# Kernel optimization log

Measured on AMD Instinct MI355X. Metric: run time of the kernel, lower is better.

The kernel has to match this reference:

```python
import jax, jax.numpy as jnp
import numpy as np
import math

B, H, T, N = 2, 4, 2048, 2048
THETA = 2.0 ** 16


def get_freqs(n: int, theta: float) -> jnp.ndarray:
    # quantize arange to multiples of 2, matching torch (t/2).floor()*2
    t = jnp.arange(n, dtype=jnp.float32)
    q = jnp.floor(t / 2.0) * 2.0
    return 1.0 / theta ** (q / n) / (2.0 * math.pi)


def rope(phases: jnp.ndarray, v: jnp.ndarray) -> jnp.ndarray:
    # v: [B,H,T,N]; phases: [T,N] (broadcast). Interleaved pair rotation.
    ph = (phases % 1.0) * (2.0 * math.pi)
    c, s = jnp.cos(ph), jnp.sin(ph)
    v2 = v.reshape(*v.shape[:-1], -1, 2)           # [...,N/2,2]
    v_rot = jnp.stack((-v2[..., 1], v2[..., 0]), axis=-1).reshape(v.shape)
    return (v * c + v_rot * s).astype(v.dtype)


def setup_inputs() -> dict:
    key = jax.random.key(0)
    kq, kv = jax.random.split(key)
    Q = jax.random.normal(kq, (B, H, T, N), dtype=jnp.float32)
    V = jax.random.normal(kv, (B, H, T, N), dtype=jnp.float32)
    return {"Q": Q, "V": V}


def reference(Q, V):
    Tlen = Q.shape[2]
    n = Q.shape[3]
    freqs = get_freqs(n, THETA)                               # [N]
    phases = jnp.arange(Tlen, dtype=jnp.float32)[:, None] * freqs[None, :]  # [T,N]
    QR = rope(phases, Q)                                      # K is Q -> KR = QR
    scores = jnp.einsum('bhtn,bhsn->bhts', QR, QR)            # [B,H,T,T]
    # strictly-causal mask: keep s < t (tril with diagonal=-1)
    mask = jnp.tril(jnp.ones((Tlen, Tlen), dtype=bool), k=-1)
    scores = jnp.where(mask, scores, 0.0)
    out = jnp.einsum('bhts,bhsn->bhtn', scores, V)
    return out
```

## Files before the change

kernel.cpp:

```cpp
#include <hip/hip_runtime.h>
#include <hip/hip_bf16.h>

#define TDIM 2048
#define NDIM 2048
#define BHN  8
#define LD   2048

typedef __attribute__((ext_vector_type(8))) short bf16x8;
typedef __attribute__((ext_vector_type(4))) float f32x4;
typedef unsigned short us;

static __device__ __forceinline__ us f2bf(float x) {
  union { __hip_bfloat16 h; us u; } cv;
  cv.h = __float2bfloat16(x);
  return cv.u;
}

__global__ __launch_bounds__(256) void rope_kernel(const float* __restrict__ Q,
                                                   us* __restrict__ QR,
                                                   int total8) {
  int idx = blockIdx.x * blockDim.x + threadIdx.x;
  if (idx >= total8) return;
  long base = (long)idx * 8;
  int n = (int)(base & (NDIM - 1));
  int t = (int)((base >> 11) & (TDIM - 1));
  const float4* p = reinterpret_cast<const float4*>(Q + base);
  float4 v0 = p[0], v1 = p[1];
  float q[8] = {v0.x, v0.y, v0.z, v0.w, v1.x, v1.y, v1.z, v1.w};
  us r[8];
  float tf = (float)t;
#pragma unroll
  for (int pr = 0; pr < 4; ++pr) {
    int nn = n + pr * 2;
    float freq = __builtin_exp2f((float)nn * (-1.0f / 128.0f)) * 0.15915494309189535f;
    float ph = tf * freq;
    ph = ph - __builtin_floorf(ph);
    float c = __builtin_amdgcn_cosf(ph);
    float s = __builtin_amdgcn_sinf(ph);
    float e = q[2 * pr], o = q[2 * pr + 1];
    r[2 * pr]     = f2bf(e * c - o * s);
    r[2 * pr + 1] = f2bf(o * c + e * s);
  }
  union { us usv[8]; bf16x8 v; } pk;
#pragma unroll
  for (int i = 0; i < 8; ++i) pk.usv[i] = r[i];
  *reinterpret_cast<bf16x8*>(QR + base) = pk.v;
}

__global__ __launch_bounds__(256) void vtrans_kernel(const float* __restrict__ V,
                                                     us* __restrict__ VT,
                                                     us* __restrict__ Sflag) {
  __shared__ float tile[32][33];
  if (Sflag != nullptr && blockIdx.x == 0 && blockIdx.y == 0 && blockIdx.z == 0 &&
      threadIdx.x == 0 && threadIdx.y == 0) {
    for (int h = 0; h < BHN; ++h) {
      unsigned* f = (unsigned*)(Sflag + (long)h * TDIM * LD + 1792);
      for (int i = 0; i < 40; ++i)
        __hip_atomic_store(&f[i], 0u, __ATOMIC_RELAXED, __HIP_MEMORY_SCOPE_AGENT);
    }
  }
  int bh = blockIdx.z;
  int n0 = blockIdx.x * 32, t0 = blockIdx.y * 32;
  const float* Vp = V + (long)bh * TDIM * NDIM;
  us* Tp = VT + (long)bh * TDIM * NDIM;
  int tx = threadIdx.x, ty = threadIdx.y;
#pragma unroll
  for (int i = 0; i < 4; ++i)
    tile[ty + i * 8][tx] = Vp[(long)(t0 + ty + i * 8) * NDIM + n0 + tx];
  __syncthreads();
#pragma unroll
  for (int i = 0; i < 4; ++i)
    Tp[(long)(n0 + ty + i * 8) * TDIM + t0 + tx] = f2bf(tile[tx][ty + i * 8]);
}

template <int PASS>
__device__ __forceinline__ void run_tile(const us* __restrict__ A,
                                         const us* __restrict__ B,
                                         void* __restrict__ Cbase,
                                         us* __restrict__ lds,
                                         int rt, int ct, int tid,
                                         unsigned* __restrict__ fh) {
  const int lane = tid & 63, wid = tid >> 6;
  const int wr = wid >> 2, wc = wid & 3;
  const int l15 = lane & 15, l4 = lane >> 4;
  const int row0 = rt * 256, col0 = ct * 256;
  const int kts = (PASS == 0) ? 32 : (rt + 1) * 4;
  const int fbase = rt * (rt + 1) / 2;

  if constexpr (PASS == 1) {
    if (wid == 0) {
      unsigned need = (1u << (rt + 1)) - 1u;
      for (;;) {
        unsigned ok = 0;
        if (lane <= rt)
          ok = (__hip_atomic_fetch_add(&fh[fbase + lane], 0u, __ATOMIC_RELAXED,
                                       __HIP_MEMORY_SCOPE_AGENT) != 0u);
        unsigned long long m = __ballot(ok);
        if (((unsigned)m & need) == need) break;
        __builtin_amdgcn_s_sleep(8);
      }
    }
    __builtin_amdgcn_s_barrier();
    asm volatile("" ::: "memory");
  }

  f32x4 acc[8][4];
#pragma unroll
  for (int m = 0; m < 8; ++m)
#pragma unroll
    for (int n = 0; n < 4; ++n) acc[m][n] = (f32x4){0.f, 0.f, 0.f, 0.f};

  auto stage = [&](int half , int t) {
    const us* g0 = (half < 2) ? A : B;
    const int tr0 = (half < 2) ? row0 : col0;
    const int h = half & 1;
    us* lb = lds + ((half < 2) ? 0 : 32768) + (t & 1) * 16384;
    const int k0 = t * 64;
#pragma unroll
    for (int r = 0; r < 2; ++r) {
      int off = r * 512 + tid;
      int row = off >> 3;
      int ch = off & 7;
      int chl = ch ^ (row & 7);
      const us* g = g0 + (long)(tr0 + h * 128 + row) * LD + (k0 + chl * 8);
      us* l = lb + h * 8192 + off * 8;
      __builtin_amdgcn_global_load_lds(
          (const __attribute__((address_space(1))) unsigned int*)g,
          (__attribute__((address_space(3))) unsigned int*)l, 16, 0, 0);
    }
  };
  auto ldA = [&](int b, int m, int ks) -> bf16x8 {
    int row = wr * 128 + m * 16 + l15;
    int ch = (ks * 4 + l4) ^ (row & 7);
    return *reinterpret_cast<const bf16x8*>(lds + b * 16384 + row * 64 + ch * 8);
  };
  auto ldB = [&](int b, int n, int ks) -> bf16x8 {
    int row = wc * 64 + n * 16 + l15;
    int ch = (ks * 4 + l4) ^ (row & 7);
    return *reinterpret_cast<const bf16x8*>(lds + 32768 + b * 16384 + row * 64 + ch * 8);
  };

  stage(0, 0); stage(1, 0); stage(2, 0); stage(3, 0);
  if (1 < kts) { stage(2, 1); stage(3, 1); }
  asm volatile("s_waitcnt vmcnt(4)" ::: "memory");
  __builtin_amdgcn_s_barrier();
  __builtin_amdgcn_sched_barrier(0);

  bf16x8 af[4][2], bfr[4][2];
  for (int t = 0; t < kts; ++t) {
    const int b = t & 1;
#pragma unroll
    for (int m = 0; m < 4; ++m) { af[m][0] = ldA(b, m, 0); af[m][1] = ldA(b, m, 1); }
#pragma unroll
    for (int n = 0; n < 2; ++n) { bfr[n][0] = ldB(b, n, 0); bfr[n][1] = ldB(b, n, 1); }
    if (t + 1 < kts) stage(0, t + 1);
    __builtin_amdgcn_s_barrier();
    asm volatile("s_waitcnt lgkmcnt(0)" ::: "memory");
    __builtin_amdgcn_sched_barrier(0);
    __builtin_amdgcn_s_setprio(1);
#pragma unroll
    for (int m = 0; m < 4; ++m)
#pragma unroll
      for (int n = 0; n < 2; ++n)
#pragma unroll
        for (int ks = 0; ks < 2; ++ks)
          acc[m][n] = __builtin_amdgcn_mfma_f32_16x16x32_bf16(af[m][ks], bfr[n][ks], acc[m][n], 0, 0, 0);
    __builtin_amdgcn_s_setprio(0);
    __builtin_amdgcn_sched_barrier(0);
    __builtin_amdgcn_s_barrier();
#pragma unroll
    for (int n = 2; n < 4; ++n) { bfr[n][0] = ldB(b, n, 0); bfr[n][1] = ldB(b, n, 1); }
    if (t + 1 < kts) stage(1, t + 1);
    __builtin_amdgcn_s_barrier();
    asm volatile("s_waitcnt lgkmcnt(0)" ::: "memory");
    __builtin_amdgcn_sched_barrier(0);
    __builtin_amdgcn_s_setprio(1);
#pragma unroll
    for (int m = 0; m < 4; ++m)
#pragma unroll
      for (int n = 2; n < 4; ++n)
#pragma unroll
        for (int ks = 0; ks < 2; ++ks)
          acc[m][n] = __builtin_amdgcn_mfma_f32_16x16x32_bf16(af[m][ks], bfr[n][ks], acc[m][n], 0, 0, 0);
    __builtin_amdgcn_s_setprio(0);
    __builtin_amdgcn_sched_barrier(0);
    __builtin_amdgcn_s_barrier();
#pragma unroll
    for (int m = 0; m < 4; ++m) { af[m][0] = ldA(b, m + 4, 0); af[m][1] = ldA(b, m + 4, 1); }
    if (t + 2 < kts) stage(2, t + 2);
    __builtin_amdgcn_s_barrier();
    asm volatile("s_waitcnt lgkmcnt(0)" ::: "memory");
    __builtin_amdgcn_sched_barrier(0);
    __builtin_amdgcn_s_setprio(1);
#pragma unroll
    for (int m = 0; m < 4; ++m)
#pragma unroll
      for (int n = 0; n < 2; ++n)
#pragma unroll
        for (int ks = 0; ks < 2; ++ks)
          acc[m + 4][n] = __builtin_amdgcn_mfma_f32_16x16x32_bf16(af[m][ks], bfr[n][ks], acc[m + 4][n], 0, 0, 0);
    __builtin_amdgcn_s_setprio(0);
    __builtin_amdgcn_sched_barrier(0);
    __builtin_amdgcn_s_barrier();
    if (t + 2 < kts) stage(3, t + 2);
    __builtin_amdgcn_s_setprio(1);
#pragma unroll
    for (int m = 0; m < 4; ++m)
#pragma unroll
      for (int n = 2; n < 4; ++n)
#pragma unroll
        for (int ks = 0; ks < 2; ++ks)
          acc[m + 4][n] = __builtin_amdgcn_mfma_f32_16x16x32_bf16(af[m][ks], bfr[n][ks], acc[m + 4][n], 0, 0, 0);
    __builtin_amdgcn_s_setprio(0);
    if (t + 2 < kts) { asm volatile("s_waitcnt vmcnt(4)" ::: "memory"); }
    else             { asm volatile("s_waitcnt vmcnt(0)" ::: "memory"); }
    __builtin_amdgcn_sched_barrier(0);
    __builtin_amdgcn_s_barrier();
    __builtin_amdgcn_sched_barrier(0);
  }

  if constexpr (PASS == 0) {
    us* C = (us*)Cbase;
    const bool diag = (rt == ct);
#pragma unroll
    for (int m = 0; m < 8; ++m) {
      int r0 = row0 + wr * 128 + m * 16 + l4 * 4;
#pragma unroll
      for (int n = 0; n < 4; ++n) {
        int cc = col0 + wc * 64 + n * 16 + l15;
#pragma unroll
        for (int j = 0; j < 4; ++j) {
          int tt = r0 + j;
          float v = acc[m][n][j];
          if (diag && cc >= tt) v = 0.0f;
          C[(long)tt * LD + cc] = f2bf(v);
        }
      }
    }
    __syncthreads();
    if (tid == 0)
      __hip_atomic_store(&fh[fbase + ct], 1u, __ATOMIC_RELEASE,
                         __HIP_MEMORY_SCOPE_AGENT);
  } else {
    float* C = (float*)Cbase;
#pragma unroll
    for (int m = 0; m < 8; ++m) {
      int r0 = row0 + wr * 128 + m * 16 + l4 * 4;
#pragma unroll
      for (int n = 0; n < 4; ++n) {
        int cc = col0 + wc * 64 + n * 16 + l15;
#pragma unroll
        for (int j = 0; j < 4; ++j)
          __builtin_nontemporal_store(acc[m][n][j], &C[(long)(r0 + j) * LD + cc]);
      }
    }
  }
}

__global__ __launch_bounds__(512, 2) void gemm_fused(const us* __restrict__ QR,
                                                     const us* __restrict__ VT,
                                                     us* __restrict__ S,
                                                     float* __restrict__ Out) {
  extern __shared__ us lds[];
  const int b = (int)blockIdx.x;
  const int head = b & 7, u = b >> 3;
  const int tid = (int)threadIdx.x;
  const us* QRh = QR + (long)head * TDIM * LD;
  const us* VTh = VT + (long)head * TDIM * LD;
  us* Sh = S + (long)head * TDIM * LD;
  float* Oh = Out + (long)head * TDIM * LD;
  unsigned* fh = (unsigned*)(Sh + 1792);
  unsigned* qc = fh + 36;

  int rt0, ct0;
  if (u < 8)       { rt0 = 7; ct0 = u; }
  else if (u < 15) { rt0 = 6; ct0 = u - 8; }
  else if (u < 21) { rt0 = 5; ct0 = u - 15; }
  else if (u < 26) { rt0 = 4; ct0 = u - 21; }
  else if (u < 30) { rt0 = 3; ct0 = u - 26; }
  else             { rt0 = 2; ct0 = (u == 30) ? 0 : 2; }
  run_tile<0>(QRh, QRh, Sh, lds, rt0, ct0, tid, fh);
  if (u >= 28) {
    int rt1, ct1;
    if (u == 28)      { rt1 = 1; ct1 = 0; }
    else if (u == 29) { rt1 = 1; ct1 = 1; }
    else if (u == 30) { rt1 = 2; ct1 = 1; }
    else              { rt1 = 0; ct1 = 0; }
    run_tile<0>(QRh, QRh, Sh, lds, rt1, ct1, tid, fh);
    run_tile<1>(Sh, VTh, Oh, lds, 1, u - 28, tid, fh);
  }

  for (;;) {
    if (tid == 0) {
      unsigned i = __hip_atomic_fetch_add(qc, 1u, __ATOMIC_RELAXED,
                                          __HIP_MEMORY_SCOPE_AGENT);
      *(volatile unsigned*)lds = i;
    }
    __syncthreads();
    unsigned i = *(volatile unsigned*)lds;
    __syncthreads();
    if (i >= 60) break;
    int rt, ct;
    if (i < 48)      { rt = 7 - (int)(i >> 3); ct = (int)(i & 7); }
    else if (i < 52) { rt = 1; ct = (int)(i - 44); }
    else             { rt = 0; ct = (int)(i - 52); }
    run_tile<1>(Sh, VTh, Oh, lds, rt, ct, tid, fh);
  }
}

template <int PASS>
__global__ __launch_bounds__(512, 2) void gemm256(
    const us* __restrict__ Abase, const us* __restrict__ Bbase,
    void* __restrict__ Cbase, int nh) {
  extern __shared__ us lds[];
  int bid = (int)blockIdx.x;
  int head, rt = 0, ct, cls = 0;
  if constexpr (PASS == 0) {
    head = bid % nh;
    int tri = bid / nh;
    rt = 0;
    while ((rt + 1) * (rt + 2) / 2 <= tri) ++rt;
    ct = tri - rt * (rt + 1) / 2;
  } else {
    head = bid % nh;
    int rem = bid / nh;
    ct = rem & 7;
    cls = rem >> 3;
  }
  const us* A = Abase + (long)head * TDIM * LD;
  const us* B = Bbase + (long)head * TDIM * LD;
  us* Sh = (us*)Cbase + (long)head * TDIM * LD;
  const int tid = (int)threadIdx.x;
  const int NSEG = (PASS == 0) ? 1 : 2;
#pragma unroll 1
  for (int seg = 0; seg < NSEG; ++seg) {
    int rts = rt, cts = ct;
    if constexpr (PASS == 1) { rts = seg ? cls : 7 - cls; cts = ct; }
    if constexpr (PASS == 0) {
      run_tile<0>(A, A, Sh, lds, rts, cts, tid, (unsigned*)(Sh + 1792));
    } else {
      float* Oh = (float*)Cbase + (long)head * TDIM * LD;
      run_tile<1>(A, B, Oh, lds, rts, cts, tid,
                  (unsigned*)((us*)Abase + (long)head * TDIM * LD + 1792));
    }
  }
}

extern "C" void kernel_launch(void* const* d_in, const int* in_sizes, int n_in,
                              void* d_out, int out_size, void* d_ws, size_t ws_size,
                              hipStream_t stream) {
  const float* Q = (const float*)d_in[0];
  const float* V = (const float*)d_in[1];
  float* Out = (float*)d_out;
  char* ws = (char*)d_ws;
  const long TN = (long)TDIM * NDIM;
  const size_t BUF = (size_t)BHN * TN * 2;
  const size_t PERBH = (size_t)TN * 2;
  const int SHMEM = 131072;

  hipFuncSetAttribute(reinterpret_cast<const void*>(&gemm_fused),
                      hipFuncAttributeMaxDynamicSharedMemorySize, SHMEM);
  hipFuncSetAttribute(reinterpret_cast<const void*>(&gemm256<0>),
                      hipFuncAttributeMaxDynamicSharedMemorySize, SHMEM);
  hipFuncSetAttribute(reinterpret_cast<const void*>(&gemm256<1>),
                      hipFuncAttributeMaxDynamicSharedMemorySize, SHMEM);

  if (ws_size >= 3 * BUF) {
    us* QRb = (us*)ws;
    us* VbT = (us*)(ws + BUF);
    us* S   = (us*)(ws + 2 * BUF);
    int total8 = (int)(BHN * TN / 8);
    rope_kernel<<<dim3(total8 / 256), dim3(256), 0, stream>>>(Q, QRb, total8);
    vtrans_kernel<<<dim3(64, 64, 8), dim3(32, 8), 0, stream>>>(V, VbT, S);
    void* args[] = {(void*)&QRb, (void*)&VbT, (void*)&S, (void*)&Out};
    hipError_t ce = hipLaunchCooperativeKernel(
        reinterpret_cast<const void*>(&gemm_fused), dim3(256), dim3(512),
        args, (unsigned)SHMEM, stream);
    if (ce != hipSuccess) {
      (void)hipGetLastError();
      gemm256<0><<<dim3(36 * BHN), dim3(512), SHMEM, stream>>>(QRb, QRb, S, BHN);
      gemm256<1><<<dim3(32 * BHN), dim3(512), SHMEM, stream>>>(S, VbT, Out, BHN);
    }
  } else {
    us* QR0 = (us*)ws;
    us* VT0 = (us*)(ws + PERBH);
    us* S0  = (us*)(ws + 2 * PERBH);
    int total8 = (int)(TN / 8);
    for (int bh = 0; bh < BHN; ++bh) {
      rope_kernel<<<dim3(total8 / 256), dim3(256), 0, stream>>>(Q + bh * TN, QR0, total8);
      vtrans_kernel<<<dim3(64, 64, 1), dim3(32, 8), 0, stream>>>(V + bh * TN, VT0, S0);
      gemm256<0><<<dim3(36), dim3(512), SHMEM, stream>>>(QR0, QR0, S0, 1);
      gemm256<1><<<dim3(32), dim3(512), SHMEM, stream>>>(S0, VT0, Out + bh * TN, 1);
    }
  }
}
```

Baseline: 259.0 us.

## Fuse RoPE and V transpose into cooperative GEMM kernel with grid sync

```diff
diff --git a/kernel.cpp b/kernel.cpp
--- a/kernel.cpp
+++ b/kernel.cpp
@@ -1,5 +1,6 @@
 #include <hip/hip_runtime.h>
 #include <hip/hip_bf16.h>
+#include <hip/hip_cooperative_groups.h>
 
 #define TDIM 2048
 #define NDIM 2048
@@ -16,15 +17,12 @@
   return cv.u;
 }
 
-__global__ __launch_bounds__(256) void rope_kernel(const float* __restrict__ Q,
-                                                   us* __restrict__ QR,
-                                                   int total8) {
-  int idx = blockIdx.x * blockDim.x + threadIdx.x;
-  if (idx >= total8) return;
-  long base = (long)idx * 8;
+static __device__ __forceinline__ void rope_unit(const float* __restrict__ Qh,
+                                                 us* __restrict__ QRh, long idx) {
+  long base = idx * 8;
   int n = (int)(base & (NDIM - 1));
-  int t = (int)((base >> 11) & (TDIM - 1));
-  const float4* p = reinterpret_cast<const float4*>(Q + base);
+  int t = (int)(base >> 11);
+  const float4* p = reinterpret_cast<const float4*>(Qh + base);
   float4 v0 = p[0], v1 = p[1];
   float q[8] = {v0.x, v0.y, v0.z, v0.w, v1.x, v1.y, v1.z, v1.w};
   us r[8];
@@ -44,21 +42,20 @@
   union { us usv[8]; bf16x8 v; } pk;
 #pragma unroll
   for (int i = 0; i < 8; ++i) pk.usv[i] = r[i];
-  *reinterpret_cast<bf16x8*>(QR + base) = pk.v;
+  *reinterpret_cast<bf16x8*>(QRh + base) = pk.v;
+}
+
+__global__ __launch_bounds__(256) void rope_kernel(const float* __restrict__ Q,
+                                                   us* __restrict__ QR,
+                                                   int total8) {
+  int idx = blockIdx.x * blockDim.x + threadIdx.x;
+  if (idx >= total8) return;
+  rope_unit(Q, QR, idx);
 }
 
 __global__ __launch_bounds__(256) void vtrans_kernel(const float* __restrict__ V,
-                                                     us* __restrict__ VT,
-                                                     us* __restrict__ Sflag) {
+                                                     us* __restrict__ VT) {
   __shared__ float tile[32][33];
-  if (Sflag != nullptr && blockIdx.x == 0 && blockIdx.y == 0 && blockIdx.z == 0 &&
-      threadIdx.x == 0 && threadIdx.y == 0) {
-    for (int h = 0; h < BHN; ++h) {
-      unsigned* f = (unsigned*)(Sflag + (long)h * TDIM * LD + 1792);
-      for (int i = 0; i < 40; ++i)
-        __hip_atomic_store(&f[i], 0u, __ATOMIC_RELAXED, __HIP_MEMORY_SCOPE_AGENT);
-    }
-  }
   int bh = blockIdx.z;
   int n0 = blockIdx.x * 32, t0 = blockIdx.y * 32;
   const float* Vp = V + (long)bh * TDIM * NDIM;
@@ -251,26 +248,61 @@
         int cc = col0 + wc * 64 + n * 16 + l15;
 #pragma unroll
         for (int j = 0; j < 4; ++j)
-          __builtin_nontemporal_store(acc[m][n][j], &C[(long)(r0 + j) * LD + cc]);
+          C[(long)(r0 + j) * LD + cc] = acc[m][n][j];
       }
     }
   }
 }
 
-__global__ __launch_bounds__(512, 2) void gemm_fused(const us* __restrict__ QR,
-                                                     const us* __restrict__ VT,
+__global__ __launch_bounds__(512, 2) void gemm_fused(const float* __restrict__ Q,
+                                                     const float* __restrict__ V,
+                                                     us* __restrict__ QR,
+                                                     us* __restrict__ VT,
                                                      us* __restrict__ S,
                                                      float* __restrict__ Out) {
   extern __shared__ us lds[];
   const int b = (int)blockIdx.x;
   const int head = b & 7, u = b >> 3;
   const int tid = (int)threadIdx.x;
-  const us* QRh = QR + (long)head * TDIM * LD;
-  const us* VTh = VT + (long)head * TDIM * LD;
-  us* Sh = S + (long)head * TDIM * LD;
-  float* Oh = Out + (long)head * TDIM * LD;
+  const long TN = (long)TDIM * NDIM;
+  const float* Qh = Q + (long)head * TN;
+  const float* Vh = V + (long)head * TN;
+  us* QRh = QR + (long)head * TN;
+  us* VTh = VT + (long)head * TN;
+  us* Sh = S + (long)head * TN;
+  float* Oh = Out + (long)head * TN;
   unsigned* fh = (unsigned*)(Sh + 1792);
   unsigned* qc = fh + 36;
+
+  if (u == 0 && tid == 0) {
+#pragma unroll
+    for (int i = 0; i < 37; ++i)
+      __hip_atomic_store(&fh[i], 0u, __ATOMIC_RELAXED, __HIP_MEMORY_SCOPE_AGENT);
+  }
+
+#pragma unroll 1
+  for (int it = 0; it < 32; ++it)
+    rope_unit(Qh, QRh, (long)(u * 512 + tid) + (long)it * 16384);
+
+  {
+    float* tile = (float*)lds;
+    const int tx = tid & 63, ty = tid >> 6;
+#pragma unroll 1
+    for (int it = 0; it < 32; ++it) {
+      int tileid = u * 32 + it;
+      int t0 = (tileid & 31) * 64, n0 = (tileid >> 5) * 64;
+      __syncthreads();
+#pragma unroll
+      for (int i = 0; i < 8; ++i)
+        tile[(ty + i * 8) * 65 + tx] = Vh[(long)(t0 + ty + i * 8) * NDIM + n0 + tx];
+      __syncthreads();
+#pragma unroll
+      for (int i = 0; i < 8; ++i)
+        VTh[(long)(n0 + ty + i * 8) * TDIM + t0 + tx] = f2bf(tile[tx * 65 + ty + i * 8]);
+    }
+  }
+
+  cooperative_groups::this_grid().sync();
 
   int rt0, ct0;
   if (u < 8)       { rt0 = 7; ct0 = u; }
@@ -369,15 +401,16 @@
     us* QRb = (us*)ws;
     us* VbT = (us*)(ws + BUF);
     us* S   = (us*)(ws + 2 * BUF);
-    int total8 = (int)(BHN * TN / 8);
-    rope_kernel<<<dim3(total8 / 256), dim3(256), 0, stream>>>(Q, QRb, total8);
-    vtrans_kernel<<<dim3(64, 64, 8), dim3(32, 8), 0, stream>>>(V, VbT, S);
-    void* args[] = {(void*)&QRb, (void*)&VbT, (void*)&S, (void*)&Out};
+    void* args[] = {(void*)&Q, (void*)&V, (void*)&QRb, (void*)&VbT,
+                    (void*)&S, (void*)&Out};
     hipError_t ce = hipLaunchCooperativeKernel(
         reinterpret_cast<const void*>(&gemm_fused), dim3(256), dim3(512),
         args, (unsigned)SHMEM, stream);
     if (ce != hipSuccess) {
       (void)hipGetLastError();
+      int total8 = (int)(BHN * TN / 8);
+      rope_kernel<<<dim3(total8 / 256), dim3(256), 0, stream>>>(Q, QRb, total8);
+      vtrans_kernel<<<dim3(64, 64, 8), dim3(32, 8), 0, stream>>>(V, VbT);
       gemm256<0><<<dim3(36 * BHN), dim3(512), SHMEM, stream>>>(QRb, QRb, S, BHN);
       gemm256<1><<<dim3(32 * BHN), dim3(512), SHMEM, stream>>>(S, VbT, Out, BHN);
     }
@@ -388,7 +421,7 @@
     int total8 = (int)(TN / 8);
     for (int bh = 0; bh < BHN; ++bh) {
       rope_kernel<<<dim3(total8 / 256), dim3(256), 0, stream>>>(Q + bh * TN, QR0, total8);
-      vtrans_kernel<<<dim3(64, 64, 1), dim3(32, 8), 0, stream>>>(V + bh * TN, VT0, S0);
+      vtrans_kernel<<<dim3(64, 64, 1), dim3(32, 8), 0, stream>>>(V + bh * TN, VT0);
       gemm256<0><<<dim3(36), dim3(512), SHMEM, stream>>>(QR0, QR0, S0, 1);
       gemm256<1><<<dim3(32), dim3(512), SHMEM, stream>>>(S0, VT0, Out + bh * TN, 1);
     }
```

New measurement: 300.6 us. 16.1% more time.
